# Kernel optimization log

Hardware: AMD Instinct MI355X
Metric: run time of the kernel (lower is better)

## Reference

```python
import jax, jax.numpy as jnp
import numpy as np

T, Z, D_DIM = 8, 2048, 1024
N_EXP, P_SLOT, H = 64, 32, 1024
LN_EPS = 1e-5


def setup_inputs() -> dict:
    key = jax.random.key(0)
    k = jax.random.split(key, 5)
    s = 0.02
    return {
        "x": jax.random.normal(k[0], (T, Z, D_DIM), dtype=jnp.float32),
        "phi_w": jax.random.normal(k[1], (N_EXP * P_SLOT, D_DIM), dtype=jnp.float32) * s,
        "phi_b": jax.random.normal(k[2], (N_EXP * P_SLOT,), dtype=jnp.float32) * s,
        "expert_w": jax.random.normal(k[3], (N_EXP, D_DIM, H), dtype=jnp.float32) * s,
        "expert_b": jax.random.normal(k[4], (N_EXP, H), dtype=jnp.float32) * s,
    }


def reference(x, phi_w, phi_b, expert_w, expert_b):
    t, z, d = x.shape
    n = expert_w.shape[0]
    p = phi_w.shape[0] // n
    # routing logits: [t, z, n, p]
    logits = (jnp.einsum('tzd,ed->tze', x, phi_w) + phi_b).reshape(t, z, n, p)
    D = jax.nn.softmax(logits, axis=3)  # dispatch: softmax over slots p
    C = jax.nn.softmax(logits, axis=2)  # combine:  softmax over experts n
    # slot inputs, summed over batch AND tokens (as in the source einsum)
    X_tilde = jnp.einsum('tznp,tzd->npd', D, x)
    X_tilde = jnp.clip(X_tilde, -33000.0, 65000.0)
    # layer norm over last dim, no affine
    mu = jnp.mean(X_tilde, axis=-1, keepdims=True)
    var = jnp.mean(jnp.square(X_tilde - mu), axis=-1, keepdims=True)
    X_tilde = (X_tilde - mu) * jax.lax.rsqrt(var + LN_EPS)
    X_tilde = jnp.tanh(X_tilde)
    # per-expert Linear, batched over experts: [n,p,d] x [n,d,H] -> [n,p,H]
    Y_tilde = jnp.einsum('npd,ndH->npH', X_tilde, expert_w) + expert_b[:, None, :]
    # combine back to tokens: [t,z,H]
    Y = jnp.einsum('tznp,npH->tzH', C, Y_tilde)
    return Y
```

## Files before the change

### kernel.cpp

```cpp
#include <hip/hip_runtime.h>
#include <hip/hip_bf16.h>
#include <math.h>

#define TOKENS   16384
#define DDIM     1024
#define NEXP     64
#define PSLOT    32
#define NSLOTS   2048
#define HDIM     1024
#define LN_EPS   1e-5f
#define KSPLIT   8

typedef __bf16 b16x8 __attribute__((ext_vector_type(8)));
typedef float  f32x4 __attribute__((ext_vector_type(4)));

__device__ __forceinline__ unsigned short f2b(float f) {
    union { float f; unsigned u; } v; v.f = f;
    unsigned r = v.u + 0x7FFF + ((v.u >> 16) & 1);
    return (unsigned short)(r >> 16);
}

__device__ __forceinline__ void load_lds16(const void* g, void* l) {
    __builtin_amdgcn_global_load_lds(
        (const __attribute__((address_space(1))) void*)g,
        (__attribute__((address_space(3))) void*)l, 16, 0, 0);
}

template<bool BIAS>
__global__ __launch_bounds__(256) void gemm_nt_bf16(
    const unsigned short* __restrict__ A,
    const unsigned short* __restrict__ B,
    const float* __restrict__ bias,
    float* __restrict__ C,
    int M, int N, int K)
{
    __shared__ unsigned short As[128 * 64];
    __shared__ unsigned short Bs[128 * 64];
    const int tid  = threadIdx.x;
    const int wave = tid >> 6;
    const int lane = tid & 63;
    const int m0 = blockIdx.y * 128;
    const int n0 = blockIdx.x * 128;
    const int wm = (wave >> 1) * 64;
    const int wn = (wave & 1) * 64;

    const int kc      = K / gridDim.z;
    const int k_begin = blockIdx.z * kc;
    const int k_end   = k_begin + kc;
    C += (size_t)blockIdx.z * M * N;

    f32x4 acc[4][4] = {};

    const int ldrow = lane >> 3;
    const int ldko  = ((lane & 7) ^ (ldrow & 7)) * 8;
    const int fr = lane & 15;
    const int fs = lane >> 4;

    for (int k0 = k_begin; k0 < k_end; k0 += 64) {
#pragma unroll
        for (int i = 0; i < 4; ++i) {
            const int chunk = wave * 4 + i;
            const int row   = chunk * 8 + ldrow;
            load_lds16(A + (size_t)(m0 + row) * K + k0 + ldko, As + chunk * 512);
            load_lds16(B + (size_t)(n0 + row) * K + k0 + ldko, Bs + chunk * 512);
        }
        __syncthreads();

#pragma unroll
        for (int h = 0; h < 2; ++h) {
            const int s = h * 4 + fs;
            b16x8 af[4], bfr[4];
#pragma unroll
            for (int i = 0; i < 4; ++i) {
                const int ma = wm + i * 16 + fr;
                const int mb = wn + i * 16 + fr;
                af[i]  = *(const b16x8*)&As[ma * 64 + (s ^ (ma & 7)) * 8];
                bfr[i] = *(const b16x8*)&Bs[mb * 64 + (s ^ (mb & 7)) * 8];
            }
#pragma unroll
            for (int i = 0; i < 4; ++i)
#pragma unroll
                for (int j = 0; j < 4; ++j)
                    acc[i][j] = __builtin_amdgcn_mfma_f32_16x16x32_bf16(
                        af[i], bfr[j], acc[i][j], 0, 0, 0);
        }
        __syncthreads();
    }

    const int col  = lane & 15;
    const int row4 = (lane >> 4) * 4;
#pragma unroll
    for (int j = 0; j < 4; ++j) {
        const int n = n0 + wn + j * 16 + col;
        const float bj = BIAS ? bias[n] : 0.f;
#pragma unroll
        for (int i = 0; i < 4; ++i) {
#pragma unroll
            for (int r = 0; r < 4; ++r) {
                const int m = m0 + wm + i * 16 + row4 + r;
                C[(size_t)m * N + n] = acc[i][j][r] + bj;
            }
        }
    }
}

__global__ __launch_bounds__(256) void prep_x(
    const float* __restrict__ in, unsigned short* __restrict__ xb,
    unsigned short* __restrict__ xT)
{
    __shared__ unsigned short tile[64][68];
    const int t  = threadIdx.x;
    const int c0 = blockIdx.x * 64;
    const int r0 = blockIdx.y * 64;
    const int tr = t >> 4, tc4 = (t & 15) * 4;
#pragma unroll
    for (int i = 0; i < 4; ++i) {
        const int r = tr + i * 16;
        const float4 v = *(const float4*)&in[(size_t)(r0 + r) * DDIM + c0 + tc4];
        ushort4 o;
        o.x = f2b(v.x); o.y = f2b(v.y); o.z = f2b(v.z); o.w = f2b(v.w);
        *(ushort4*)&xb[(size_t)(r0 + r) * DDIM + c0 + tc4] = o;
        tile[tc4 + 0][r] = o.x; tile[tc4 + 1][r] = o.y;
        tile[tc4 + 2][r] = o.z; tile[tc4 + 3][r] = o.w;
    }
    __syncthreads();
#pragma unroll
    for (int i = 0; i < 4; ++i) {
        const int r = tr + i * 16;
        ushort4 o;
        o.x = tile[r][tc4 + 0]; o.y = tile[r][tc4 + 1];
        o.z = tile[r][tc4 + 2]; o.w = tile[r][tc4 + 3];
        *(ushort4*)&xT[(size_t)(c0 + r) * TOKENS + r0 + tc4] = o;
    }
}

__global__ __launch_bounds__(256) void cast_f32_bf16(
    const float* __restrict__ in, unsigned short* __restrict__ out)
{
    const size_t i = (size_t)(blockIdx.x * 256 + threadIdx.x) * 8;
    const float4 a = *(const float4*)&in[i];
    const float4 b = *(const float4*)&in[i + 4];
    ushort4 o0, o1;
    o0.x = f2b(a.x); o0.y = f2b(a.y); o0.z = f2b(a.z); o0.w = f2b(a.w);
    o1.x = f2b(b.x); o1.y = f2b(b.y); o1.z = f2b(b.z); o1.w = f2b(b.w);
    *(ushort4*)&out[i]     = o0;
    *(ushort4*)&out[i + 4] = o1;
}

template<typename TIN>
__global__ __launch_bounds__(256) void transpose_cast(
    const TIN* __restrict__ in, unsigned short* __restrict__ out, int R, int C)
{
    __shared__ unsigned short tile[64][68];
    const int t  = threadIdx.x;
    const int r0 = blockIdx.y * 64, c0 = blockIdx.x * 64;
    const int tr = t >> 4, tc4 = (t & 15) * 4;
#pragma unroll
    for (int i = 0; i < 4; ++i) {
        const int r = tr + i * 16;
        const TIN* p = in + (size_t)(r0 + r) * C + c0 + tc4;
        if constexpr (sizeof(TIN) == 4) {
            const float4 v = *(const float4*)p;
            tile[tc4 + 0][r] = f2b(v.x); tile[tc4 + 1][r] = f2b(v.y);
            tile[tc4 + 2][r] = f2b(v.z); tile[tc4 + 3][r] = f2b(v.w);
        } else {
            const ushort4 v = *(const ushort4*)p;
            tile[tc4 + 0][r] = v.x; tile[tc4 + 1][r] = v.y;
            tile[tc4 + 2][r] = v.z; tile[tc4 + 3][r] = v.w;
        }
    }
    __syncthreads();
#pragma unroll
    for (int i = 0; i < 4; ++i) {
        const int r = tr + i * 16;
        ushort4 o;
        o.x = tile[r][tc4 + 0]; o.y = tile[r][tc4 + 1];
        o.z = tile[r][tc4 + 2]; o.w = tile[r][tc4 + 3];
        *(ushort4*)&out[(size_t)(c0 + r) * R + r0 + tc4] = o;
    }
}

__global__ __launch_bounds__(256) void softmax_dc(
    const float* __restrict__ logits,
    unsigned short* __restrict__ Db, unsigned short* __restrict__ Cb)
{
    __shared__ float ls[NEXP * 33];
    __shared__ float dmax[NEXP], dinv[NEXP];
    __shared__ float cmax[PSLOT], cinv[PSLOT];
    const int tid = threadIdx.x;
    const size_t base = (size_t)blockIdx.x * NSLOTS;

#pragma unroll
    for (int i = 0; i < 8; ++i) {
        const int e = tid + i * 256;
        ls[e + (e >> 5)] = logits[base + e];
    }
    __syncthreads();

    if (tid < 64) {
        const float* r = &ls[tid * 33];
        float m = r[0];
#pragma unroll
        for (int p = 1; p < PSLOT; ++p) m = fmaxf(m, r[p]);
        float s = 0.f;
#pragma unroll
        for (int p = 0; p < PSLOT; ++p) s += __expf(r[p] - m);
        dmax[tid] = m; dinv[tid] = 1.f / s;
    } else if (tid < 96) {
        const int p = tid - 64;
        float m = ls[p];
#pragma unroll
        for (int n = 1; n < NEXP; ++n) m = fmaxf(m, ls[n * 33 + p]);
        float s = 0.f;
#pragma unroll
        for (int n = 0; n < NEXP; ++n) s += __expf(ls[n * 33 + p] - m);
        cmax[p] = m; cinv[p] = 1.f / s;
    }
    __syncthreads();

#pragma unroll
    for (int i = 0; i < 8; ++i) {
        const int e = tid + i * 256;
        const int n = e >> 5, p = e & 31;
        const float l = ls[e + n];
        Db[base + e] = f2b(__expf(l - dmax[n]) * dinv[n]);
        Cb[base + e] = f2b(__expf(l - cmax[p]) * cinv[p]);
    }
}

__global__ __launch_bounds__(256) void reduce_ln_tanh(
    const float* __restrict__ parts, float* __restrict__ Xt)
{
    const int tid = threadIdx.x;
    const size_t off = (size_t)blockIdx.x * DDIM + tid * 4;
    __shared__ float red1[4], red2[4];

    float4 v = *(const float4*)&parts[off];
#pragma unroll
    for (int s = 1; s < KSPLIT; ++s) {
        const float4 p = *(const float4*)&parts[(size_t)s * NSLOTS * DDIM + off];
        v.x += p.x; v.y += p.y; v.z += p.z; v.w += p.w;
    }
    v.x = fminf(fmaxf(v.x, -33000.f), 65000.f);
    v.y = fminf(fmaxf(v.y, -33000.f), 65000.f);
    v.z = fminf(fmaxf(v.z, -33000.f), 65000.f);
    v.w = fminf(fmaxf(v.w, -33000.f), 65000.f);

    float s = v.x + v.y + v.z + v.w;
#pragma unroll
    for (int off2 = 32; off2 > 0; off2 >>= 1) s += __shfl_down(s, off2);
    if ((tid & 63) == 0) red1[tid >> 6] = s;
    __syncthreads();
    const float mu = (red1[0] + red1[1] + red1[2] + red1[3]) * (1.f / DDIM);

    const float dx = v.x - mu, dy = v.y - mu, dz = v.z - mu, dw = v.w - mu;
    float q = dx * dx + dy * dy + dz * dz + dw * dw;
#pragma unroll
    for (int off2 = 32; off2 > 0; off2 >>= 1) q += __shfl_down(q, off2);
    if ((tid & 63) == 0) red2[tid >> 6] = q;
    __syncthreads();
    const float var = (red2[0] + red2[1] + red2[2] + red2[3]) * (1.f / DDIM);
    const float sc = rsqrtf(var + LN_EPS);

    float4 o;
    o.x = tanhf(dx * sc); o.y = tanhf(dy * sc);
    o.z = tanhf(dz * sc); o.w = tanhf(dw * sc);
    *(float4*)&Xt[off] = o;
}

__global__ __launch_bounds__(256) void expert_gemm(
    const float* __restrict__ Xt, const float* __restrict__ W,
    const float* __restrict__ bias, float* __restrict__ Yt)
{
    const int n   = blockIdx.y;
    const int h0  = blockIdx.x * 64;
    const int tid = threadIdx.x;
    __shared__ float As[32][17];
    __shared__ float Bs[16][68];

    const int r  = tid >> 3;
    const int c8 = (tid & 7) * 8;
    float acc[8];
#pragma unroll
    for (int j = 0; j < 8; ++j) acc[j] = 0.f;

    const float* Wn = W + (size_t)n * DDIM * HDIM;
    for (int k0 = 0; k0 < DDIM; k0 += 16) {
        if (tid < 128) {
            const int row = tid >> 2, c4 = (tid & 3) * 4;
            const float4 v = *(const float4*)&Xt[(size_t)(n * 32 + row) * DDIM + k0 + c4];
            As[row][c4 + 0] = v.x; As[row][c4 + 1] = v.y;
            As[row][c4 + 2] = v.z; As[row][c4 + 3] = v.w;
        }
        {
            const int row = tid >> 4, c4 = (tid & 15) * 4;
            *(float4*)&Bs[row][c4] =
                *(const float4*)&Wn[(size_t)(k0 + row) * HDIM + h0 + c4];
        }
        __syncthreads();
#pragma unroll
        for (int kk = 0; kk < 16; ++kk) {
            const float a = As[r][kk];
            const float4 b0 = *(const float4*)&Bs[kk][c8];
            const float4 b1 = *(const float4*)&Bs[kk][c8 + 4];
            acc[0] = fmaf(a, b0.x, acc[0]); acc[1] = fmaf(a, b0.y, acc[1]);
            acc[2] = fmaf(a, b0.z, acc[2]); acc[3] = fmaf(a, b0.w, acc[3]);
            acc[4] = fmaf(a, b1.x, acc[4]); acc[5] = fmaf(a, b1.y, acc[5]);
            acc[6] = fmaf(a, b1.z, acc[6]); acc[7] = fmaf(a, b1.w, acc[7]);
        }
        __syncthreads();
    }

    float4 o0, o1;
    const float* bn = bias + (size_t)n * HDIM + h0 + c8;
    o0.x = acc[0] + bn[0]; o0.y = acc[1] + bn[1];
    o0.z = acc[2] + bn[2]; o0.w = acc[3] + bn[3];
    o1.x = acc[4] + bn[4]; o1.y = acc[5] + bn[5];
    o1.z = acc[6] + bn[6]; o1.w = acc[7] + bn[7];
    float* outp = Yt + (size_t)(n * 32 + r) * HDIM + h0 + c8;
    *(float4*)&outp[0] = o0;
    *(float4*)&outp[4] = o1;
}

extern "C" void kernel_launch(void* const* d_in, const int* in_sizes, int n_in,
                              void* d_out, int out_size, void* d_ws, size_t ws_size,
                              hipStream_t stream)
{
    const float* x        = (const float*)d_in[0];
    const float* phi_w    = (const float*)d_in[1];
    const float* phi_b    = (const float*)d_in[2];
    const float* expert_w = (const float*)d_in[3];
    const float* expert_b = (const float*)d_in[4];
    float* out = (float*)d_out;

    char* ws = (char*)d_ws;
    const size_t MB = 1u << 20;
    unsigned short* xb     = (unsigned short*)(ws);
    unsigned short* xT     = (unsigned short*)(ws +  32 * MB);
    unsigned short* pwb    = (unsigned short*)(ws +  64 * MB);
    float*          logits = (float*)(ws +  68 * MB);
    unsigned short* Db     = (unsigned short*)(ws + 196 * MB);
    unsigned short* Cb     = (unsigned short*)(ws + 260 * MB);
    unsigned short* DbT    = (unsigned short*)(ws + 324 * MB);
    float*          parts  = (float*)(ws + 388 * MB);
    float*          Xt     = (float*)(ws + 452 * MB);
    float*          Yt     = (float*)(ws + 460 * MB);
    unsigned short* YtT    = (unsigned short*)(ws + 468 * MB);

    prep_x<<<dim3(DDIM / 64, TOKENS / 64), 256, 0, stream>>>(x, xb, xT);
    cast_f32_bf16<<<NSLOTS * DDIM / (256 * 8), 256, 0, stream>>>(phi_w, pwb);

    gemm_nt_bf16<true><<<dim3(NSLOTS / 128, TOKENS / 128), 256, 0, stream>>>(
        xb, pwb, phi_b, logits, TOKENS, NSLOTS, DDIM);

    softmax_dc<<<TOKENS, 256, 0, stream>>>(logits, Db, Cb);

    transpose_cast<unsigned short><<<dim3(NSLOTS / 64, TOKENS / 64), 256, 0, stream>>>(
        Db, DbT, TOKENS, NSLOTS);

    gemm_nt_bf16<false>
        <<<dim3(DDIM / 128, NSLOTS / 128, KSPLIT), 256, 0, stream>>>(
            DbT, xT, nullptr, parts, NSLOTS, DDIM, TOKENS);

    reduce_ln_tanh<<<NSLOTS, 256, 0, stream>>>(parts, Xt);

    expert_gemm<<<dim3(HDIM / 64, NEXP), 256, 0, stream>>>(
        Xt, expert_w, expert_b, Yt);

    transpose_cast<float><<<dim3(HDIM / 64, NSLOTS / 64), 256, 0, stream>>>(
        Yt, YtT, NSLOTS, HDIM);

    gemm_nt_bf16<false><<<dim3(HDIM / 128, TOKENS / 128), 256, 0, stream>>>(
        Cb, YtT, nullptr, out, TOKENS, HDIM, NSLOTS);
}
```

Measured before the change: 895.1 us.

## Replace bf16 GEMM with 256x256 double-buffered, interleaved-prefetch MFMA kernel

Replaces the 128x128 single-buffer GEMM with a 256x256-tile, 512-thread kernel. It double-buffers LDS and interleaves global-to-LDS prefetch of the next K tile with quarter-tile MFMA groups, using explicit barriers, vmcnt waits and setprio. The larger tiles raise data reuse per LDS load, and the staging hides memory latency behind compute. In exchange, the grids shrink (for example the split-K GEMM drops to 4x8x8 blocks), which may underfill the CUs. The prefetch clamp also requires an even tile count per split.

```diff
diff --git a/kernel.cpp b/kernel.cpp
--- a/kernel.cpp
+++ b/kernel.cpp
@@ -27,81 +27,132 @@
 }
 
 template<bool BIAS>
-__global__ __launch_bounds__(256) void gemm_nt_bf16(
+__global__ __launch_bounds__(512, 2) void gemm_nt_256(
     const unsigned short* __restrict__ A,
     const unsigned short* __restrict__ B,
     const float* __restrict__ bias,
     float* __restrict__ C,
     int M, int N, int K)
 {
-    __shared__ unsigned short As[128 * 64];
-    __shared__ unsigned short Bs[128 * 64];
+    __shared__ unsigned short lds[2][2][256 * 64];
     const int tid  = threadIdx.x;
     const int wave = tid >> 6;
     const int lane = tid & 63;
-    const int m0 = blockIdx.y * 128;
-    const int n0 = blockIdx.x * 128;
-    const int wm = (wave >> 1) * 64;
-    const int wn = (wave & 1) * 64;
-
-    const int kc      = K / gridDim.z;
-    const int k_begin = blockIdx.z * kc;
-    const int k_end   = k_begin + kc;
-    C += (size_t)blockIdx.z * M * N;
-
-    f32x4 acc[4][4] = {};
-
-    const int ldrow = lane >> 3;
-    const int ldko  = ((lane & 7) ^ (ldrow & 7)) * 8;
+    const int wr = wave >> 2;
+    const int wc = wave & 3;
     const int fr = lane & 15;
     const int fs = lane >> 4;
-
-    for (int k0 = k_begin; k0 < k_end; k0 += 64) {
-#pragma unroll
-        for (int i = 0; i < 4; ++i) {
-            const int chunk = wave * 4 + i;
-            const int row   = chunk * 8 + ldrow;
-            load_lds16(A + (size_t)(m0 + row) * K + k0 + ldko, As + chunk * 512);
-            load_lds16(B + (size_t)(n0 + row) * K + k0 + ldko, Bs + chunk * 512);
-        }
-        __syncthreads();
-
-#pragma unroll
-        for (int h = 0; h < 2; ++h) {
-            const int s = h * 4 + fs;
-            b16x8 af[4], bfr[4];
-#pragma unroll
-            for (int i = 0; i < 4; ++i) {
-                const int ma = wm + i * 16 + fr;
-                const int mb = wn + i * 16 + fr;
-                af[i]  = *(const b16x8*)&As[ma * 64 + (s ^ (ma & 7)) * 8];
-                bfr[i] = *(const b16x8*)&Bs[mb * 64 + (s ^ (mb & 7)) * 8];
-            }
-#pragma unroll
-            for (int i = 0; i < 4; ++i)
-#pragma unroll
-                for (int j = 0; j < 4; ++j)
-                    acc[i][j] = __builtin_amdgcn_mfma_f32_16x16x32_bf16(
-                        af[i], bfr[j], acc[i][j], 0, 0, 0);
-        }
-        __syncthreads();
+    const int kswz = ((lane & 7) ^ (lane >> 3)) * 8;
+    const int m0 = blockIdx.y * 256;
+    const int n0 = blockIdx.x * 256;
+
+    const int kc = K / gridDim.z;
+    const int kb = blockIdx.z * kc;
+    C += (size_t)blockIdx.z * M * N;
+    const int NT = kc >> 6;
+
+    f32x4 acc[8][4] = {};
+    b16x8 Ag[4][2], Bf[2][2], Bs2[2][2];
+
+#define KOF(T)   (kb + ((T) < NT ? (T) : (NT - 1)) * 64)
+
+#define STAGE_A(BUF, T, R0) { \
+    const int k0_ = KOF(T); \
+    _Pragma("unroll") for (int hh = 0; hh < 2; ++hh) { \
+        const int rp_ = (R0) + hh * 64 + wave * 8 + (lane >> 3); \
+        const int L_  = ((rp_ >> 6) & 1) * 128 + ((rp_ >> 7) & 1) * 64 + (rp_ & 63); \
+        load_lds16(A + (size_t)(m0 + L_) * K + k0_ + kswz, \
+                   &lds[BUF][0][((R0) + hh * 64 + wave * 8) * 64]); } }
+
+#define STAGE_B(BUF, T, R0) { \
+    const int k0_ = KOF(T); \
+    _Pragma("unroll") for (int hh = 0; hh < 2; ++hh) { \
+        const int rp_ = (R0) + hh * 64 + wave * 8 + (lane >> 3); \
+        const int L_  = ((rp_ >> 5) & 3) * 64 + ((rp_ >> 7) & 1) * 32 + (rp_ & 31); \
+        load_lds16(B + (size_t)(n0 + L_) * K + k0_ + kswz, \
+                   &lds[BUF][1][((R0) + hh * 64 + wave * 8) * 64]); } }
+
+#define LDA_G(BUF, IBASE) \
+    _Pragma("unroll") for (int ii = 0; ii < 4; ++ii) { \
+        const int rp_ = (IBASE) + 64 * wr + ii * 16 + fr; \
+        _Pragma("unroll") for (int h = 0; h < 2; ++h) \
+            Ag[ii][h] = *(const b16x8*)&lds[BUF][0][rp_ * 64 + (((h * 4 + fs) ^ (rp_ & 7)) * 8)]; }
+
+#define LDB_G(BUF, JBASE, DST) \
+    _Pragma("unroll") for (int jj = 0; jj < 2; ++jj) { \
+        const int rp_ = (JBASE) + 32 * wc + jj * 16 + fr; \
+        _Pragma("unroll") for (int h = 0; h < 2; ++h) \
+            DST[jj][h] = *(const b16x8*)&lds[BUF][1][rp_ * 64 + (((h * 4 + fs) ^ (rp_ & 7)) * 8)]; }
+
+#define MFMA_Q(IB, JB, BREG) \
+    __builtin_amdgcn_s_setprio(1); \
+    _Pragma("unroll") for (int ii = 0; ii < 4; ++ii) \
+    _Pragma("unroll") for (int jj = 0; jj < 2; ++jj) \
+    _Pragma("unroll") for (int h = 0; h < 2; ++h) \
+        acc[(IB) + ii][(JB) + jj] = __builtin_amdgcn_mfma_f32_16x16x32_bf16( \
+            Ag[ii][h], BREG[jj][h], acc[(IB) + ii][(JB) + jj], 0, 0, 0); \
+    __builtin_amdgcn_s_setprio(0);
+
+#define BAR1  { __builtin_amdgcn_s_barrier(); __builtin_amdgcn_sched_barrier(0); }
+#define BAR2  { __builtin_amdgcn_s_barrier(); }
+#define VMW6  { asm volatile("s_waitcnt vmcnt(6)" ::: "memory"); \
+                __builtin_amdgcn_sched_barrier(0); }
+
+    STAGE_A(0, 0, 0);   STAGE_B(0, 0, 0);   STAGE_B(0, 0, 128);  STAGE_A(0, 0, 128);
+    STAGE_A(1, 1, 0);   STAGE_B(1, 1, 0);   STAGE_B(1, 1, 128);
+    VMW6; BAR2;
+
+    const int nit = NT >> 1;
+    for (int it = 0; it < nit; ++it) {
+        const int t1 = 2 * it + 1;
+        LDA_G(0, 0); LDB_G(0, 0, Bf);
+        STAGE_A(1, t1, 128);
+        BAR1; MFMA_Q(0, 0, Bf); BAR2;
+        LDB_G(0, 128, Bs2);
+        STAGE_A(0, t1 + 1, 0);
+        BAR1; MFMA_Q(0, 2, Bs2); BAR2;
+        LDA_G(0, 128);
+        STAGE_B(0, t1 + 1, 0);
+        BAR1; MFMA_Q(4, 2, Bs2); BAR2;
+        STAGE_B(0, t1 + 1, 128);
+        BAR1; MFMA_Q(4, 0, Bf); VMW6; BAR2;
+        LDA_G(1, 0); LDB_G(1, 0, Bf);
+        STAGE_A(0, t1 + 1, 128);
+        BAR1; MFMA_Q(0, 0, Bf); BAR2;
+        LDB_G(1, 128, Bs2);
+        STAGE_A(1, t1 + 2, 0);
+        BAR1; MFMA_Q(0, 2, Bs2); BAR2;
+        LDA_G(1, 128);
+        STAGE_B(1, t1 + 2, 0);
+        BAR1; MFMA_Q(4, 2, Bs2); BAR2;
+        STAGE_B(1, t1 + 2, 128);
+        BAR1; MFMA_Q(4, 0, Bf); VMW6; BAR2;
     }
 
     const int col  = lane & 15;
     const int row4 = (lane >> 4) * 4;
 #pragma unroll
     for (int j = 0; j < 4; ++j) {
-        const int n = n0 + wn + j * 16 + col;
+        const int n = n0 + wc * 64 + j * 16 + col;
         const float bj = BIAS ? bias[n] : 0.f;
 #pragma unroll
-        for (int i = 0; i < 4; ++i) {
+        for (int i = 0; i < 8; ++i) {
 #pragma unroll
             for (int r = 0; r < 4; ++r) {
-                const int m = m0 + wm + i * 16 + row4 + r;
+                const int m = m0 + wr * 128 + i * 16 + row4 + r;
                 C[(size_t)m * N + n] = acc[i][j][r] + bj;
             }
         }
     }
+#undef KOF
+#undef STAGE_A
+#undef STAGE_B
+#undef LDA_G
+#undef LDB_G
+#undef MFMA_Q
+#undef BAR1
+#undef BAR2
+#undef VMW6
 }
 
 __global__ __launch_bounds__(256) void prep_x(
@@ -350,7 +401,7 @@
     prep_x<<<dim3(DDIM / 64, TOKENS / 64), 256, 0, stream>>>(x, xb, xT);
     cast_f32_bf16<<<NSLOTS * DDIM / (256 * 8), 256, 0, stream>>>(phi_w, pwb);
 
-    gemm_nt_bf16<true><<<dim3(NSLOTS / 128, TOKENS / 128), 256, 0, stream>>>(
+    gemm_nt_256<true><<<dim3(NSLOTS / 256, TOKENS / 256), 512, 0, stream>>>(
         xb, pwb, phi_b, logits, TOKENS, NSLOTS, DDIM);
 
     softmax_dc<<<TOKENS, 256, 0, stream>>>(logits, Db, Cb);
@@ -358,8 +409,8 @@
     transpose_cast<unsigned short><<<dim3(NSLOTS / 64, TOKENS / 64), 256, 0, stream>>>(
         Db, DbT, TOKENS, NSLOTS);
 
-    gemm_nt_bf16<false>
-        <<<dim3(DDIM / 128, NSLOTS / 128, KSPLIT), 256, 0, stream>>>(
+    gemm_nt_256<false>
+        <<<dim3(DDIM / 256, NSLOTS / 256, KSPLIT), 512, 0, stream>>>(
             DbT, xT, nullptr, parts, NSLOTS, DDIM, TOKENS);
 
     reduce_ln_tanh<<<NSLOTS, 256, 0, stream>>>(parts, Xt);
@@ -370,6 +421,6 @@
     transpose_cast<float><<<dim3(HDIM / 64, NSLOTS / 64), 256, 0, stream>>>(
         Yt, YtT, NSLOTS, HDIM);
 
-    gemm_nt_bf16<false><<<dim3(HDIM / 128, TOKENS / 128), 256, 0, stream>>>(
+    gemm_nt_256<false><<<dim3(HDIM / 256, TOKENS / 256), 512, 0, stream>>>(
         Cb, YtT, nullptr, out, TOKENS, HDIM, NSLOTS);
 }
```

Measured after the change: 773.2 us. -13.6%, faster.
